# Kernel optimization log

Hardware: AMD Instinct MI355X
Metric: run time of the kernel (lower is better)

Reference implementation:

```python
import jax, jax.numpy as jnp
import numpy as np

SQRT_D = 8.0

def setup_inputs() -> dict:
    key = jax.random.key(0)
    kq, kk, kv = jax.random.split(key, 3)
    shape = (2, 16, 2048, 64)  # [batch, heads, seq, head_dim]
    return {
        "q": jax.random.normal(kq, shape, dtype=jnp.float32),
        "k": jax.random.normal(kk, shape, dtype=jnp.float32),
        "v": jax.random.normal(kv, shape, dtype=jnp.float32),
    }

def reference(q, k, v):
    # score = softmax(QK^T / sqrt_d) over the key axis j
    scores = jnp.einsum('bhif,bhjf->bhij', q, k) / SQRT_D
    probs = jax.nn.softmax(scores, axis=-1)
    # Note: original returns output permuted to [b, i, h, f]
    attn = jnp.einsum('bhij,bhjf->bihf', probs, v)
    return attn
```

## Files before the change

### kernel.cpp

```cpp
#include <hip/hip_runtime.h>

#define S_LEN 2048
#define HEADS 16
#define DIM 64

typedef __attribute__((ext_vector_type(8))) short short8;
typedef __attribute__((ext_vector_type(16))) float float16v;
typedef __attribute__((ext_vector_type(4))) float float4v;
typedef __attribute__((ext_vector_type(4))) unsigned uint4v;

static __device__ __forceinline__ unsigned pkbf(float lo, float hi) {
  unsigned r;
  asm("v_cvt_pk_bf16_f32 %0, %1, %2" : "=v"(r) : "v"(lo), "v"(hi));
  return r;
}

static __device__ __forceinline__ void gll16(const short* g, short* l) {
  __builtin_amdgcn_global_load_lds(
      (const __attribute__((address_space(1))) void*)g,
      (__attribute__((address_space(3))) void*)l, 16, 0, 0);
}

__global__ __launch_bounds__(256) void prep(const float* __restrict__ kk,
                                            const float* __restrict__ vv,
                                            short* __restrict__ kb,
                                            short* __restrict__ vt) {
  __shared__ unsigned t32[64 * 36];
  const int bx = blockIdx.x;
  const int bh = bx >> 5;
  const int j0 = (bx & 31) * 64;
  const int tid = threadIdx.x;

  {
    const int j = tid >> 2, f0 = (tid & 3) * 16;
    const float4v* src = (const float4v*)(kk + ((size_t)bh * S_LEN + j0 + j) * DIM + f0);
    float4v a0 = src[0], a1 = src[1], a2 = src[2], a3 = src[3];
    uint4v w0, w1;
    w0[0] = pkbf(a0[0], a0[1]); w0[1] = pkbf(a0[2], a0[3]);
    w0[2] = pkbf(a1[0], a1[1]); w0[3] = pkbf(a1[2], a1[3]);
    w1[0] = pkbf(a2[0], a2[1]); w1[1] = pkbf(a2[2], a2[3]);
    w1[2] = pkbf(a3[0], a3[1]); w1[3] = pkbf(a3[2], a3[3]);
    uint4v* dst = (uint4v*)(kb + ((size_t)bh * S_LEN + j0 + j) * DIM + f0);
    dst[0] = w0; dst[1] = w1;
  }
  {
    const int m = tid & 31, f0 = (tid >> 5) * 8;
    const float* r0 = vv + ((size_t)bh * S_LEN + j0 + m) * DIM + f0;
    const float* r1 = r0 + 32 * DIM;
    float4v a0 = *(const float4v*)r0, a1 = *(const float4v*)(r0 + 4);
    float4v b0 = *(const float4v*)r1, b1 = *(const float4v*)(r1 + 4);
#pragma unroll
    for (int e = 0; e < 4; e++) {
      t32[(f0 + e) * 36 + m] = pkbf(a0[e], b0[e]);
      t32[(f0 + 4 + e) * 36 + m] = pkbf(a1[e], b1[e]);
    }
  }
  __syncthreads();
  {
    const int f = tid >> 2, pp = (tid & 3) * 8;
    uint4v c0 = *(const uint4v*)&t32[f * 36 + pp];
    uint4v c1 = *(const uint4v*)&t32[f * 36 + pp + 4];
    uint4v* dst = (uint4v*)(vt + ((size_t)bh * DIM + f) * S_LEN + j0 + pp * 2);
    dst[0] = c0; dst[1] = c1;
  }
}

__global__ __launch_bounds__(128, 2) void attn_fwd(const float* __restrict__ q,
                                                   const short* __restrict__ kb,
                                                   const short* __restrict__ vt,
                                                   float* __restrict__ out) {
  __shared__ short k_lds[64 * 64];
  __shared__ short v_lds[64 * 64];
  __shared__ unsigned p_lds[2][32 * 36];

  const int bx = blockIdx.x;
  const int bh = bx >> 5, it = bx & 31;
  const int b = bh >> 4, h = bh & 15;
  const int tid = threadIdx.x;
  const int w = tid >> 6, lane = tid & 63;
  const int n = lane & 31, half = lane >> 5;
  const int i0 = it * 64 + w * 32;

  short8 qa[4];
  {
    const float* qrow = q + ((size_t)bh * S_LEN + i0 + n) * DIM + half * 8;
#pragma unroll
    for (int ks = 0; ks < 4; ks++) {
      float4v x0 = *(const float4v*)(qrow + ks * 16);
      float4v x1 = *(const float4v*)(qrow + ks * 16 + 4);
      uint4v pk;
      pk[0] = pkbf(x0[0] * 0.125f, x0[1] * 0.125f);
      pk[1] = pkbf(x0[2] * 0.125f, x0[3] * 0.125f);
      pk[2] = pkbf(x1[0] * 0.125f, x1[1] * 0.125f);
      pk[3] = pkbf(x1[2] * 0.125f, x1[3] * 0.125f);
      qa[ks] = *(short8*)&pk;
    }
  }

  float16v acc0, acc1;
  float lp[16];
#pragma unroll
  for (int e = 0; e < 16; e++) { acc0[e] = 0.f; acc1[e] = 0.f; lp[e] = 0.f; }

  const short* kbase = kb + (size_t)bh * S_LEN * DIM;
  const short* vbase = vt + (size_t)bh * DIM * S_LEN;
  unsigned* const pw = p_lds[w];

  for (int j0 = 0; j0 < S_LEN; j0 += 64) {
    __syncthreads();
#pragma unroll
    for (int qi = 0; qi < 4; qi++) {
      const int ib = w * 4 + qi;
      const int jl = ib * 8 + (lane >> 3);
      const int ch = (lane & 7) ^ (jl & 7);
      gll16(kbase + (size_t)(j0 + jl) * DIM + ch * 8, &k_lds[ib * 512]);
      gll16(vbase + (size_t)jl * S_LEN + j0 + ch * 8, &v_lds[ib * 512]);
    }
    __syncthreads();

    float16v s0, s1;
#pragma unroll
    for (int e = 0; e < 16; e++) { s0[e] = 0.f; s1[e] = 0.f; }
#pragma unroll
    for (int ks = 0; ks < 4; ks++) {
      const int g = ks * 2 + half;
      const int sw = g ^ (n & 7);
      short8 kf0 = *(const short8*)&k_lds[(n * 8 + sw) * 8];
      short8 kf1 = *(const short8*)&k_lds[((32 + n) * 8 + sw) * 8];
      s0 = __builtin_amdgcn_mfma_f32_32x32x16_bf16(qa[ks], kf0, s0, 0, 0, 0);
      s1 = __builtin_amdgcn_mfma_f32_32x32x16_bf16(qa[ks], kf1, s1, 0, 0, 0);
    }

#pragma unroll
    for (int rg = 0; rg < 16; rg++) {
      const float e0 = __expf(s0[rg]);
      const float e1 = __expf(s1[rg]);
      lp[rg] += e0 + e1;
      const int row = (rg & 3) + 8 * (rg >> 2) + 4 * half;
      pw[row * 36 + n] = pkbf(e0, e1);
    }

#pragma unroll
    for (int ks = 0; ks < 4; ks++) {
      short8 pa = *(const short8*)((const short*)&pw[n * 36 + ks * 8 + half * 4]);
      const int g = ks * 2 + half;
      const int sw = g ^ (n & 7);
      short8 vf0 = *(const short8*)&v_lds[(n * 8 + sw) * 8];
      short8 vf1 = *(const short8*)&v_lds[((32 + n) * 8 + sw) * 8];
      acc0 = __builtin_amdgcn_mfma_f32_32x32x16_bf16(pa, vf0, acc0, 0, 0, 0);
      acc1 = __builtin_amdgcn_mfma_f32_32x32x16_bf16(pa, vf1, acc1, 0, 0, 0);
    }
  }

#pragma unroll
  for (int rg = 0; rg < 16; rg++) {
    float t = lp[rg];
    t += __shfl_xor(t, 1);
    t += __shfl_xor(t, 2);
    t += __shfl_xor(t, 4);
    t += __shfl_xor(t, 8);
    t += __shfl_xor(t, 16);
    const float inv = 1.f / t;
    const int row = (rg & 3) + 8 * (rg >> 2) + 4 * half;
    float* dst = out + (((size_t)b * S_LEN + i0 + row) * HEADS + h) * DIM;
    dst[n] = acc0[rg] * inv;
    dst[n + 32] = acc1[rg] * inv;
  }
}

extern "C" void kernel_launch(void* const* d_in, const int* in_sizes, int n_in,
                              void* d_out, int out_size, void* d_ws, size_t ws_size,
                              hipStream_t stream) {
  const float* q = (const float*)d_in[0];
  const float* k = (const float*)d_in[1];
  const float* v = (const float*)d_in[2];
  float* out = (float*)d_out;
  short* kb = (short*)d_ws;
  short* vt = (short*)d_ws + (size_t)32 * S_LEN * DIM;

  prep<<<1024, 256, 0, stream>>>(k, v, kb, vt);
  attn_fwd<<<1024, 128, 0, stream>>>(q, kb, vt, out);
}
```

Measured before the change: 145.8 us.

## Compute transposed S^T so P stays in registers, drop LDS round-trip

The QK^T MFMA now runs with operands swapped so each lane holds scores for one query row across keys. The exponentiated probabilities can then be packed to bf16 directly in registers as the A/B operand of the PV MFMA, removing the per-tile P write/read through LDS and its layout shuffle. The row-sum reduction collapses to a single scalar with one final shuffle. The output is staged through LDS for coalesced float4 stores, and the V transpose in prep is permuted to match the new key ordering. This relies on the key permutation in V being exactly consistent with the MFMA register layout.

```diff
diff --git a/kernel.cpp b/kernel.cpp
--- a/kernel.cpp
+++ b/kernel.cpp
@@ -25,7 +25,7 @@
                                             const float* __restrict__ vv,
                                             short* __restrict__ kb,
                                             short* __restrict__ vt) {
-  __shared__ unsigned t32[64 * 36];
+  __shared__ unsigned t32[64 * 33];
   const int bx = blockIdx.x;
   const int bh = bx >> 5;
   const int j0 = (bx & 31) * 64;
@@ -44,23 +44,24 @@
     dst[0] = w0; dst[1] = w1;
   }
   {
-    const int m = tid & 31, f0 = (tid >> 5) * 8;
-    const float* r0 = vv + ((size_t)bh * S_LEN + j0 + m) * DIM + f0;
-    const float* r1 = r0 + 32 * DIM;
+    const int jp = (tid & 31) * 2, f0 = (tid >> 5) * 8;
+    const int pp = ((jp & ~12) | ((jp & 4) << 1) | ((jp & 8) >> 1)) >> 1;
+    const float* r0 = vv + ((size_t)bh * S_LEN + j0 + jp) * DIM + f0;
+    const float* r1 = r0 + DIM;
     float4v a0 = *(const float4v*)r0, a1 = *(const float4v*)(r0 + 4);
     float4v b0 = *(const float4v*)r1, b1 = *(const float4v*)(r1 + 4);
 #pragma unroll
     for (int e = 0; e < 4; e++) {
-      t32[(f0 + e) * 36 + m] = pkbf(a0[e], b0[e]);
-      t32[(f0 + 4 + e) * 36 + m] = pkbf(a1[e], b1[e]);
+      t32[(f0 + e) * 33 + pp]     = pkbf(a0[e], b0[e]);
+      t32[(f0 + 4 + e) * 33 + pp] = pkbf(a1[e], b1[e]);
     }
   }
   __syncthreads();
   {
-    const int f = tid >> 2, pp = (tid & 3) * 8;
-    uint4v c0 = *(const uint4v*)&t32[f * 36 + pp];
-    uint4v c1 = *(const uint4v*)&t32[f * 36 + pp + 4];
-    uint4v* dst = (uint4v*)(vt + ((size_t)bh * DIM + f) * S_LEN + j0 + pp * 2);
+    const int f = tid >> 2, x0 = (tid & 3) * 8;
+    uint4v c0 = *(const uint4v*)&t32[f * 33 + x0];
+    uint4v c1 = *(const uint4v*)&t32[f * 33 + x0 + 4];
+    uint4v* dst = (uint4v*)(vt + ((size_t)bh * DIM + f) * S_LEN + j0 + x0 * 2);
     dst[0] = c0; dst[1] = c1;
   }
 }
@@ -69,42 +70,41 @@
                                                    const short* __restrict__ kb,
                                                    const short* __restrict__ vt,
                                                    float* __restrict__ out) {
-  __shared__ short k_lds[64 * 64];
-  __shared__ short v_lds[64 * 64];
-  __shared__ unsigned p_lds[2][32 * 36];
+  __shared__ alignas(16) float smem[64 * 68];
+  short* const k_lds = (short*)smem;
+  short* const v_lds = k_lds + 4096;
 
   const int bx = blockIdx.x;
   const int bh = bx >> 5, it = bx & 31;
   const int b = bh >> 4, h = bh & 15;
   const int tid = threadIdx.x;
   const int w = tid >> 6, lane = tid & 63;
-  const int n = lane & 31, half = lane >> 5;
+  const int n = lane & 31, hf = lane >> 5;
   const int i0 = it * 64 + w * 32;
 
   short8 qa[4];
   {
-    const float* qrow = q + ((size_t)bh * S_LEN + i0 + n) * DIM + half * 8;
+    const float* qrow = q + ((size_t)bh * S_LEN + i0 + n) * DIM + hf * 8;
 #pragma unroll
     for (int ks = 0; ks < 4; ks++) {
       float4v x0 = *(const float4v*)(qrow + ks * 16);
       float4v x1 = *(const float4v*)(qrow + ks * 16 + 4);
-      uint4v pk;
-      pk[0] = pkbf(x0[0] * 0.125f, x0[1] * 0.125f);
-      pk[1] = pkbf(x0[2] * 0.125f, x0[3] * 0.125f);
-      pk[2] = pkbf(x1[0] * 0.125f, x1[1] * 0.125f);
-      pk[3] = pkbf(x1[2] * 0.125f, x1[3] * 0.125f);
-      qa[ks] = *(short8*)&pk;
+      uint4v pk_;
+      pk_[0] = pkbf(x0[0] * 0.125f, x0[1] * 0.125f);
+      pk_[1] = pkbf(x0[2] * 0.125f, x0[3] * 0.125f);
+      pk_[2] = pkbf(x1[0] * 0.125f, x1[1] * 0.125f);
+      pk_[3] = pkbf(x1[2] * 0.125f, x1[3] * 0.125f);
+      qa[ks] = *(short8*)&pk_;
     }
   }
 
   float16v acc0, acc1;
-  float lp[16];
 #pragma unroll
-  for (int e = 0; e < 16; e++) { acc0[e] = 0.f; acc1[e] = 0.f; lp[e] = 0.f; }
+  for (int e = 0; e < 16; e++) { acc0[e] = 0.f; acc1[e] = 0.f; }
+  float lp = 0.f;
 
   const short* kbase = kb + (size_t)bh * S_LEN * DIM;
   const short* vbase = vt + (size_t)bh * DIM * S_LEN;
-  unsigned* const pw = p_lds[w];
 
   for (int j0 = 0; j0 < S_LEN; j0 += 64) {
     __syncthreads();
@@ -118,53 +118,69 @@
     }
     __syncthreads();
 
-    float16v s0, s1;
+    float16v st0, st1;
 #pragma unroll
-    for (int e = 0; e < 16; e++) { s0[e] = 0.f; s1[e] = 0.f; }
+    for (int e = 0; e < 16; e++) { st0[e] = 0.f; st1[e] = 0.f; }
 #pragma unroll
     for (int ks = 0; ks < 4; ks++) {
-      const int g = ks * 2 + half;
-      const int sw = g ^ (n & 7);
-      short8 kf0 = *(const short8*)&k_lds[(n * 8 + sw) * 8];
-      short8 kf1 = *(const short8*)&k_lds[((32 + n) * 8 + sw) * 8];
-      s0 = __builtin_amdgcn_mfma_f32_32x32x16_bf16(qa[ks], kf0, s0, 0, 0, 0);
-      s1 = __builtin_amdgcn_mfma_f32_32x32x16_bf16(qa[ks], kf1, s1, 0, 0, 0);
+      const int cpos = (2 * ks + hf) ^ (n & 7);
+      short8 kf0 = *(const short8*)&k_lds[(n * 8 + cpos) * 8];
+      short8 kf1 = *(const short8*)&k_lds[((32 + n) * 8 + cpos) * 8];
+      st0 = __builtin_amdgcn_mfma_f32_32x32x16_bf16(kf0, qa[ks], st0, 0, 0, 0);
+      st1 = __builtin_amdgcn_mfma_f32_32x32x16_bf16(kf1, qa[ks], st1, 0, 0, 0);
     }
 
 #pragma unroll
-    for (int rg = 0; rg < 16; rg++) {
-      const float e0 = __expf(s0[rg]);
-      const float e1 = __expf(s1[rg]);
-      lp[rg] += e0 + e1;
-      const int row = (rg & 3) + 8 * (rg >> 2) + 4 * half;
-      pw[row * 36 + n] = pkbf(e0, e1);
+    for (int e = 0; e < 16; e++) {
+      st0[e] = __expf(st0[e]);
+      st1[e] = __expf(st1[e]);
+      lp += st0[e] + st1[e];
+    }
+
+    uint4v pb[4];
+#pragma unroll
+    for (int u = 0; u < 4; u++) {
+      pb[0][u] = pkbf(st0[2 * u], st0[2 * u + 1]);
+      pb[1][u] = pkbf(st0[8 + 2 * u], st0[8 + 2 * u + 1]);
+      pb[2][u] = pkbf(st1[2 * u], st1[2 * u + 1]);
+      pb[3][u] = pkbf(st1[8 + 2 * u], st1[8 + 2 * u + 1]);
     }
 
 #pragma unroll
-    for (int ks = 0; ks < 4; ks++) {
-      short8 pa = *(const short8*)((const short*)&pw[n * 36 + ks * 8 + half * 4]);
-      const int g = ks * 2 + half;
-      const int sw = g ^ (n & 7);
-      short8 vf0 = *(const short8*)&v_lds[(n * 8 + sw) * 8];
-      short8 vf1 = *(const short8*)&v_lds[((32 + n) * 8 + sw) * 8];
-      acc0 = __builtin_amdgcn_mfma_f32_32x32x16_bf16(pa, vf0, acc0, 0, 0, 0);
-      acc1 = __builtin_amdgcn_mfma_f32_32x32x16_bf16(pa, vf1, acc1, 0, 0, 0);
+    for (int c = 0; c < 4; c++) {
+      const int cpos = (2 * c + hf) ^ (n & 7);
+      short8 vf0 = *(const short8*)&v_lds[(n * 8 + cpos) * 8];
+      short8 vf1 = *(const short8*)&v_lds[((32 + n) * 8 + cpos) * 8];
+      short8 pa = *(short8*)&pb[c];
+      acc0 = __builtin_amdgcn_mfma_f32_32x32x16_bf16(vf0, pa, acc0, 0, 0, 0);
+      acc1 = __builtin_amdgcn_mfma_f32_32x32x16_bf16(vf1, pa, acc1, 0, 0, 0);
     }
   }
 
+  const float tot = lp + __shfl_xor(lp, 32);
+  const float inv = 1.f / tot;
+
+  __syncthreads();
+  float* const ob = smem;
 #pragma unroll
-  for (int rg = 0; rg < 16; rg++) {
-    float t = lp[rg];
-    t += __shfl_xor(t, 1);
-    t += __shfl_xor(t, 2);
-    t += __shfl_xor(t, 4);
-    t += __shfl_xor(t, 8);
-    t += __shfl_xor(t, 16);
-    const float inv = 1.f / t;
-    const int row = (rg & 3) + 8 * (rg >> 2) + 4 * half;
-    float* dst = out + (((size_t)b * S_LEN + i0 + row) * HEADS + h) * DIM;
-    dst[n] = acc0[rg] * inv;
-    dst[n + 32] = acc1[rg] * inv;
+  for (int a = 0; a < 4; a++) {
+    float4v t0, t1;
+#pragma unroll
+    for (int e = 0; e < 4; e++) {
+      t0[e] = acc0[4 * a + e] * inv;
+      t1[e] = acc1[4 * a + e] * inv;
+    }
+    const int row = w * 32 + n;
+    *(float4v*)&ob[row * 68 + 8 * a + 4 * hf] = t0;
+    *(float4v*)&ob[row * 68 + 32 + 8 * a + 4 * hf] = t1;
+  }
+  __syncthreads();
+  {
+    const int il = tid >> 1, fq = (tid & 1) * 32;
+    const float* src = &ob[il * 68 + fq];
+    float* dst = out + (((size_t)b * S_LEN + it * 64 + il) * HEADS + h) * DIM + fq;
+#pragma unroll
+    for (int u = 0; u < 8; u++) ((float4v*)dst)[u] = ((const float4v*)src)[u];
   }
 }
 
```

New measurement: 145.5 us. Within noise of the previous version (-0.2%).
